# Optimization experiments

Measured on AMD Instinct MI355X. Metric: run time of the kernel, lower is better.

## Reference

```python
import jax, jax.numpy as jnp
import numpy as np

B, N, DIM = 16, 1024, 512
H, DH = 8, 64
INNER = H * DH            # 512
FF = 4 * DIM              # 2048
CIN = 2 * DIM             # conv inner dim = dim*expansion_factor = 1024
K = 31                    # depthwise kernel size
MAXPOS = 512
EPS = 1e-5


def layernorm(x, g, b):
    mu = jnp.mean(x, axis=-1, keepdims=True)
    var = jnp.mean(jnp.square(x - mu), axis=-1, keepdims=True)
    return (x - mu) * jax.lax.rsqrt(var + EPS) * g + b


def swish(x):
    return x * jax.nn.sigmoid(x)


def feed_forward(x, w1, b1, w2, b2):
    h = swish(x @ w1 + b1)
    return h @ w2 + b2


def setup_inputs() -> dict:
    key = jax.random.key(0)
    ks = jax.random.split(key, 16)
    s = 0.02
    w = lambda k, shape: (jax.random.normal(k, shape, jnp.float32) * s)
    inp = {
        "x": jax.random.normal(ks[0], (B, N, DIM), jnp.float32),
        # FF1
        "ff1_ln_g": jnp.ones((DIM,), jnp.float32), "ff1_ln_b": jnp.zeros((DIM,), jnp.float32),
        "ff1_w1": w(ks[1], (DIM, FF)), "ff1_b1": jnp.zeros((FF,), jnp.float32),
        "ff1_w2": w(ks[2], (FF, DIM)), "ff1_b2": jnp.zeros((DIM,), jnp.float32),
        # Attention (PreNorm)
        "attn_ln_g": jnp.ones((DIM,), jnp.float32), "attn_ln_b": jnp.zeros((DIM,), jnp.float32),
        "wq": w(ks[3], (DIM, INNER)),
        "wkv": w(ks[4], (DIM, 2 * INNER)),
        "wo": w(ks[5], (INNER, DIM)), "bo": jnp.zeros((DIM,), jnp.float32),
        "rel_emb": w(ks[6], (2 * MAXPOS + 1, DH)),
        # Conv module
        "conv_ln_g": jnp.ones((DIM,), jnp.float32), "conv_ln_b": jnp.zeros((DIM,), jnp.float32),
        "conv1_w": w(ks[7], (DIM, 2 * CIN)), "conv1_b": jnp.zeros((2 * CIN,), jnp.float32),
        "dw_w": w(ks[8], (CIN, 1, K)), "dw_b": jnp.zeros((CIN,), jnp.float32),
        "conv2_w": w(ks[9], (CIN, DIM)), "conv2_b": jnp.zeros((DIM,), jnp.float32),
        # FF2
        "ff2_ln_g": jnp.ones((DIM,), jnp.float32), "ff2_ln_b": jnp.zeros((DIM,), jnp.float32),
        "ff2_w1": w(ks[10], (DIM, FF)), "ff2_b1": jnp.zeros((FF,), jnp.float32),
        "ff2_w2": w(ks[11], (FF, DIM)), "ff2_b2": jnp.zeros((DIM,), jnp.float32),
        # post norm
        "post_ln_g": jnp.ones((DIM,), jnp.float32), "post_ln_b": jnp.zeros((DIM,), jnp.float32),
    }
    return inp


def attention(x, wq, wkv, wo, bo, rel_emb):
    b, n, _ = x.shape
    scale = DH ** -0.5
    q = (x @ wq).reshape(b, n, H, DH).transpose(0, 2, 1, 3)   # b h n d
    kv = x @ wkv
    k = kv[..., :INNER].reshape(b, n, H, DH).transpose(0, 2, 1, 3)
    v = kv[..., INNER:].reshape(b, n, H, DH).transpose(0, 2, 1, 3)
    dots = jnp.einsum("bhid,bhjd->bhij", q, k) * scale
    # relative positional bias via embedding lookup
    seq = jnp.arange(n)
    dist = jnp.clip(seq[:, None] - seq[None, :], -MAXPOS, MAXPOS) + MAXPOS  # [n, n]
    rel = jnp.take(rel_emb, dist, axis=0)                      # [n, n, d]
    pos = jnp.einsum("bhnd,njd->bhnj", q, rel) * scale
    attn = jax.nn.softmax(dots + pos, axis=-1)
    out = jnp.einsum("bhij,bhjd->bhid", attn, v)
    out = out.transpose(0, 2, 1, 3).reshape(b, n, INNER)
    return out @ wo + bo


def conv_module(x, ln_g, ln_b, conv1_w, conv1_b, dw_w, dw_b, conv2_w, conv2_b):
    h = layernorm(x, ln_g, ln_b)                               # [b, n, dim]
    h = h @ conv1_w + conv1_b                                  # pointwise conv -> [b, n, 2*CIN]
    a, g = h[..., :CIN], h[..., CIN:]
    h = a * jax.nn.sigmoid(g)                                  # GLU (channel dim)
    hc = h.transpose(0, 2, 1)                                  # [b, CIN, n]
    hc = jnp.pad(hc, ((0, 0), (0, 0), (K - 1, 0)))             # causal left pad
    hc = jax.lax.conv_general_dilated(
        hc, dw_w, window_strides=(1,), padding="VALID",
        feature_group_count=CIN, dimension_numbers=("NCH", "OIH", "NCH"),
    ) + dw_b[None, :, None]
    h = hc.transpose(0, 2, 1)                                  # [b, n, CIN]
    h = swish(h)
    return h @ conv2_w + conv2_b


def reference(x, ff1_ln_g, ff1_ln_b, ff1_w1, ff1_b1, ff1_w2, ff1_b2,
              attn_ln_g, attn_ln_b, wq, wkv, wo, bo, rel_emb,
              conv_ln_g, conv_ln_b, conv1_w, conv1_b, dw_w, dw_b, conv2_w, conv2_b,
              ff2_ln_g, ff2_ln_b, ff2_w1, ff2_b1, ff2_w2, ff2_b2,
              post_ln_g, post_ln_b):
    x = 0.5 * feed_forward(layernorm(x, ff1_ln_g, ff1_ln_b), ff1_w1, ff1_b1, ff1_w2, ff1_b2) + x
    x = attention(layernorm(x, attn_ln_g, attn_ln_b), wq, wkv, wo, bo, rel_emb) + x
    x = conv_module(x, conv_ln_g, conv_ln_b, conv1_w, conv1_b, dw_w, dw_b, conv2_w, conv2_b) + x
    x = 0.5 * feed_forward(layernorm(x, ff2_ln_g, ff2_ln_b), ff2_w1, ff2_b1, ff2_w2, ff2_b2) + x
    return layernorm(x, post_ln_g, post_ln_b)
```

## Files before the change

kernel.cpp:

```cpp
#include <hip/hip_runtime.h>


#define BN 16384

typedef unsigned short u16;
typedef __attribute__((ext_vector_type(8))) __bf16 bf16x8;
typedef __attribute__((ext_vector_type(4))) float f32x4;
typedef __attribute__((ext_vector_type(8))) unsigned short u16x8;

__device__ __forceinline__ float sigf(float x) { return 1.f / (1.f + __expf(-x)); }
__device__ __forceinline__ u16 f2bf(float f) {
  unsigned int u = __float_as_uint(f);
  u += 0x7FFF + ((u >> 16) & 1);
  return (u16)(u >> 16);
}
__device__ __forceinline__ u16 f2bfn(float f) {
  const __bf16 h = (__bf16)f;
  return __builtin_bit_cast(u16, h);
}
__device__ __forceinline__ float bf2f(u16 u) {
  return __uint_as_float(((unsigned int)u) << 16);
}
__device__ __forceinline__ void gl_lds16(const void* g, void* lds) {
  __builtin_amdgcn_global_load_lds(
      (const __attribute__((address_space(1))) unsigned int*)g,
      (__attribute__((address_space(3))) unsigned int*)lds, 16, 0, 0);
}

__global__ __launch_bounds__(256) void ln_kernel(const float* __restrict__ in,
    const float* __restrict__ g, const float* __restrict__ b,
    u16* outb, float* outf) {
  const int t = threadIdx.x;
  const int row = blockIdx.x * 2 + (t >> 7);
  const int tl = t & 127;
  const float4 v = ((const float4*)(in + (size_t)row * 512))[tl];
  float s = v.x + v.y + v.z + v.w;
  float sq = v.x * v.x + v.y * v.y + v.z * v.z + v.w * v.w;
#pragma unroll
  for (int o = 32; o > 0; o >>= 1) {
    s += __shfl_down(s, o);
    sq += __shfl_down(sq, o);
  }
  __shared__ float ss[4], ssq[4];
  if ((t & 63) == 0) { ss[t >> 6] = s; ssq[t >> 6] = sq; }
  __syncthreads();
  const int base = (t >> 7) * 2;
  s = ss[base] + ss[base + 1];
  sq = ssq[base] + ssq[base + 1];
  const float mu = s * (1.f / 512.f);
  const float var = fmaxf(sq * (1.f / 512.f) - mu * mu, 0.f);
  const float rstd = rsqrtf(var + 1e-5f);
  const float4 gg = ((const float4*)g)[tl];
  const float4 bb = ((const float4*)b)[tl];
  float o0 = (v.x - mu) * rstd * gg.x + bb.x;
  float o1 = (v.y - mu) * rstd * gg.y + bb.y;
  float o2 = (v.z - mu) * rstd * gg.z + bb.z;
  float o3 = (v.w - mu) * rstd * gg.w + bb.w;
  if (outf) {
    float4 o4 = {o0, o1, o2, o3};
    ((float4*)(outf + (size_t)row * 512))[tl] = o4;
  } else {
    ushort4 u4 = {f2bf(o0), f2bf(o1), f2bf(o2), f2bf(o3)};
    ((ushort4*)(outb + (size_t)row * 512))[tl] = u4;
  }
}

__global__ __launch_bounds__(256) void wtrans(const float* __restrict__ W,
                                              u16* __restrict__ WT, int K, int N) {
  const int n0 = blockIdx.x * 32, k0 = blockIdx.y * 32;
  const int t = threadIdx.x;
  const int tx = t & 31, ty = t >> 5;
  __shared__ float T[32][33];
#pragma unroll
  for (int i = 0; i < 4; ++i)
    T[tx][ty + 8 * i] = W[(size_t)(k0 + ty + 8 * i) * N + n0 + tx];
  __syncthreads();
#pragma unroll
  for (int i = 0; i < 4; ++i)
    WT[(size_t)(n0 + ty + 8 * i) * K + k0 + tx] = f2bf(T[ty + 8 * i][tx]);
}

__global__ __launch_bounds__(256) void cvt_bf16(const float* __restrict__ in,
                                                u16* __restrict__ out, int n) {
  const int i = blockIdx.x * 256 + threadIdx.x;
  if (i < n) out[i] = f2bf(in[i]);
}

__global__ __launch_bounds__(512) void gemm256(const u16* __restrict__ A,
    const u16* __restrict__ WT, const float* __restrict__ bias,
    u16* __restrict__ Cb, int K, int ldc, int act) {
  __shared__ __align__(16) u16 LDSB[65536];
  u16* const As0 = LDSB;
  u16* const As1 = LDSB + 16384;
  u16* const Bs0 = LDSB + 32768;
  u16* const Bs1 = LDSB + 49152;
  const int t = threadIdx.x;
  int bx = blockIdx.x, by = blockIdx.y;
  {
    const int nx = gridDim.x;
    const int lin = bx + nx * by;
    const int xcd = lin & 7;
    const int s = lin >> 3;
    const int ny8 = gridDim.y >> 3;
    const int sy = s / nx;
    by = xcd * ny8 + sy;
    bx = s - sy * nx;
  }
  const int n0 = bx * 256;
  const int m0 = by * 256;
  const int w = t >> 6;
  const int wr = w >> 2, wc = w & 3;
  const int lc = t & 15, lq = (t >> 4) & 3;

  f32x4 acc[8][4];
#pragma unroll
  for (int i = 0; i < 8; ++i)
#pragma unroll
    for (int j = 0; j < 4; ++j)
#pragma unroll
      for (int r = 0; r < 4; ++r) acc[i][j][r] = 0.f;

  int sfr[4], sfc[4];
#pragma unroll
  for (int s = 0; s < 4; ++s) {
    const int f = t + 512 * s;
    sfr[s] = f >> 3;
    sfc[s] = ((f & 7) ^ (sfr[s] & 7)) * 8;
  }

  auto STAGE = [&](u16* Ad, u16* Bd, int kt) {
#pragma unroll
    for (int s = 0; s < 4; ++s) {
      gl_lds16(&A[(size_t)(m0 + sfr[s]) * K + kt + sfc[s]], &Ad[(t + 512 * s) * 8]);
      gl_lds16(&WT[(size_t)(n0 + sfr[s]) * K + kt + sfc[s]], &Bd[(t + 512 * s) * 8]);
    }
  };

  auto COMPUTE = [&](const u16* Asrc, const u16* Bsrc) {
#pragma unroll
    for (int kk = 0; kk < 2; ++kk) {
      const int koff = ((kk * 4 + lq) ^ (lc & 7)) * 8;
      bf16x8 bfr[4];
#pragma unroll
      for (int j = 0; j < 4; ++j)
        bfr[j] = *(const bf16x8*)&Bsrc[(wc * 64 + j * 16 + lc) * 64 + koff];
#pragma unroll
      for (int i = 0; i < 8; ++i) {
        const bf16x8 af = *(const bf16x8*)&Asrc[(wr * 128 + i * 16 + lc) * 64 + koff];
#pragma unroll
        for (int j = 0; j < 4; ++j)
          acc[i][j] = __builtin_amdgcn_mfma_f32_16x16x32_bf16(af, bfr[j], acc[i][j], 0, 0, 0);
      }
    }
  };

  STAGE(As0, Bs0, 0);
  __syncthreads();

  for (int kt2 = 0; kt2 < K; kt2 += 128) {
    STAGE(As1, Bs1, kt2 + 64);
    COMPUTE(As0, Bs0);
    __syncthreads();
    if (kt2 + 128 < K) STAGE(As0, Bs0, kt2 + 128);
    COMPUTE(As1, Bs1);
    __syncthreads();
  }

#pragma unroll
  for (int j = 0; j < 4; ++j) {
    const int coll = wc * 64 + j * 16 + lc;
    const float bj = bias[n0 + coll];
#pragma unroll
    for (int i = 0; i < 8; ++i) {
      const int rowl0 = wr * 128 + i * 16 + lq * 4;
#pragma unroll
      for (int r = 0; r < 4; ++r) {
        float v = acc[i][j][r] + bj;
        if (act) v = v * sigf(v);
        LDSB[(rowl0 + r) * 256 + coll] = f2bfn(v);
      }
    }
  }
  __syncthreads();
#pragma unroll
  for (int vv = 0; vv < 16; ++vv) {
    const int e = t + 512 * vv;
    *(u16x8*)&Cb[(size_t)(m0 + (e >> 5)) * ldc + n0 + (e & 31) * 8] =
        *(const u16x8*)&LDSB[e * 8];
  }
}

__global__ __launch_bounds__(256) void gemm_bf16(const u16* __restrict__ A,
    const u16* __restrict__ WT, const float* __restrict__ bias,
    const float* res, float* Cf, u16* Cb, u16* VTout, int K, int N, int ldc,
    float alpha, int act, int qn, int vt0) {
  __shared__ __align__(16) u16 Ast[128 * 64];
  __shared__ __align__(16) u16 Bst[128 * 64];
  const int t = threadIdx.x;
  int bx = blockIdx.x, by = blockIdx.y;
  {
    const int nx = gridDim.x;
    const int lin = bx + nx * by;
    const int xcd = lin & 7;
    const int s = lin >> 3;
    const int ny8 = gridDim.y >> 3;
    const int sy = s / nx;
    by = xcd * ny8 + sy;
    bx = s - sy * nx;
  }
  const int n0 = bx * 128;
  const int m0 = by * 128;
  const int w = t >> 6;
  const int lc = t & 15, lq = (t >> 4) & 3;
  const int wy = w >> 1, wx = w & 1;
  f32x4 acc[4][4];
#pragma unroll
  for (int i = 0; i < 4; ++i)
#pragma unroll
    for (int j = 0; j < 4; ++j)
#pragma unroll
      for (int r = 0; r < 4; ++r) acc[i][j][r] = 0.f;

  const int koff0 = (lq ^ (lc & 7)) * 8;
  const int koff1 = ((4 + lq) ^ (lc & 7)) * 8;

  for (int kt = 0; kt < K; kt += 64) {
#pragma unroll
    for (int s = 0; s < 4; ++s) {
      const int f = t + 256 * s;
      const int fr = f >> 3;
      const int fc = (f & 7) ^ (fr & 7);
      gl_lds16(&A[(size_t)(m0 + fr) * K + kt + fc * 8], &Ast[f * 8]);
      gl_lds16(&WT[(size_t)(n0 + fr) * K + kt + fc * 8], &Bst[f * 8]);
    }
    __syncthreads();
#pragma unroll
    for (int kk = 0; kk < 2; ++kk) {
      const int koff = kk ? koff1 : koff0;
      bf16x8 bfr[4];
#pragma unroll
      for (int j = 0; j < 4; ++j)
        bfr[j] = *(const bf16x8*)&Bst[(wx * 64 + j * 16 + lc) * 64 + koff];
#pragma unroll
      for (int i = 0; i < 4; ++i) {
        const bf16x8 af = *(const bf16x8*)&Ast[(wy * 64 + i * 16 + lc) * 64 + koff];
#pragma unroll
        for (int j = 0; j < 4; ++j)
          acc[i][j] = __builtin_amdgcn_mfma_f32_16x16x32_bf16(af, bfr[j], acc[i][j], 0, 0, 0);
      }
    }
    __syncthreads();
  }

  const bool vtblk = (VTout != nullptr) && (n0 >= vt0);
  if (Cb && !vtblk) {
#pragma unroll
    for (int j = 0; j < 4; ++j) {
      const int coll = wx * 64 + j * 16 + lc;
      const float bj = bias ? bias[n0 + coll] : 0.f;
      const float al = ((n0 + coll) < qn) ? alpha : 1.f;
#pragma unroll
      for (int i = 0; i < 4; ++i) {
        const int rowl0 = wy * 64 + i * 16 + lq * 4;
#pragma unroll
        for (int r = 0; r < 4; ++r) {
          float v = acc[i][j][r] + bj;
          if (act) v = v * sigf(v);
          v *= al;
          const int rowl = rowl0 + r;
          u16* cl = (rowl < 64) ? &Ast[rowl * 128] : &Bst[(rowl - 64) * 128];
          cl[coll] = f2bfn(v);
        }
      }
    }
    __syncthreads();
#pragma unroll
    for (int vv = 0; vv < 8; ++vv) {
      const int e = t + 256 * vv;
      const int rowl = e >> 4;
      const int col = (e & 15) * 8;
      const u16* cl = (rowl < 64) ? &Ast[rowl * 128] : &Bst[(rowl - 64) * 128];
      const u16x8 val = *(const u16x8*)&cl[col];
      *(u16x8*)&Cb[(size_t)(m0 + rowl) * ldc + n0 + col] = val;
    }
    return;
  }

#pragma unroll
  for (int j = 0; j < 4; ++j) {
    const int col = n0 + wx * 64 + j * 16 + lc;
    const float bj = bias ? bias[col] : 0.f;
    const float al = (col < qn) ? alpha : 1.f;
    const bool vtc = vtblk && (col >= vt0);
#pragma unroll
    for (int i = 0; i < 4; ++i) {
      const int row0 = m0 + wy * 64 + i * 16 + lq * 4;
      float v4[4];
#pragma unroll
      for (int r = 0; r < 4; ++r) {
        float v = acc[i][j][r] + bj;
        if (act) v = v * sigf(v);
        v *= al;
        if (res) v += res[(size_t)(row0 + r) * ldc + col];
        v4[r] = v;
      }
      if (vtc) {
        const int cm = col - vt0;
        const int hh = cm >> 6, dd = cm & 63;
        const int bb = row0 >> 10, nl = row0 & 1023;
        ushort4 o4 = {f2bfn(v4[0]), f2bfn(v4[1]), f2bfn(v4[2]), f2bfn(v4[3])};
        *(ushort4*)&VTout[((size_t)((bb * 8 + hh) * 64 + dd)) * 1024 + nl] = o4;
      } else {
#pragma unroll
        for (int r = 0; r < 4; ++r) {
          const size_t off = (size_t)(row0 + r) * ldc + col;
          if (Cf) Cf[off] = v4[r];
          else Cb[off] = f2bfn(v4[r]);
        }
      }
    }
  }
}

__global__ __launch_bounds__(256) void attn_mfma(const u16* __restrict__ QKV,
    const u16* __restrict__ Vt, const u16* __restrict__ Rb, u16* __restrict__ O) {
  const int lin = blockIdx.x;
  const int hb = lin & 127;
  const int n0 = (lin >> 7) * 64;
  const int h = hb & 7, b = hb >> 3;
  const int t = threadIdx.x;
  const int w = t >> 6;
  const int lc = t & 15, lq = (t >> 4) & 3;

  __shared__ __align__(16) u16 Ks[2][64 * 64];
  __shared__ __align__(16) u16 Vs[2][64 * 64];
  __shared__ __align__(16) u16 SP[64 * 72];

  bf16x8 qf[2];
  {
    const size_t qrow = (size_t)(b * 1024 + n0 + w * 16 + lc) * 1536 + h * 64;
    qf[0] = *(const bf16x8*)&QKV[qrow + lq * 8];
    qf[1] = *(const bf16x8*)&QKV[qrow + 32 + lq * 8];
  }

  const u16* Kg = QKV + (size_t)b * 1024 * 1536 + 512 + h * 64;
  const u16* Vg = Vt + (size_t)(b * 8 + h) * 64 * 1024;

  const int srow = t >> 3;
  const int scb0 = ((t & 7) ^ (srow & 7)) * 8;
  const int srow1 = (t + 256) >> 3;
  const int scb1 = (((t + 256) & 7) ^ (srow1 & 7)) * 8;

  gl_lds16(&Kg[(size_t)srow * 1536 + scb0], &Ks[0][t * 8]);
  gl_lds16(&Vg[(size_t)srow * 1024 + scb0], &Vs[0][t * 8]);
  gl_lds16(&Kg[(size_t)srow1 * 1536 + scb1], &Ks[0][(t + 256) * 8]);
  gl_lds16(&Vg[(size_t)srow1 * 1024 + scb1], &Vs[0][(t + 256) * 8]);

  float l_r[4] = {0.f, 0.f, 0.f, 0.f};
  f32x4 o[4];
#pragma unroll
  for (int dt = 0; dt < 4; ++dt)
#pragma unroll
    for (int r = 0; r < 4; ++r) o[dt][r] = 0.f;

  const int swz0 = (lq ^ (lc & 7)) * 8;
  const int swz1 = ((4 + lq) ^ (lc & 7)) * 8;

  int buf = 0;
  for (int jt = 0; jt < 16; ++jt) {
    const int j0 = jt * 64;
    __syncthreads();

    if (jt < 15) {
      const int j1 = j0 + 64;
      gl_lds16(&Kg[(size_t)(j1 + srow) * 1536 + scb0], &Ks[buf ^ 1][t * 8]);
      gl_lds16(&Vg[(size_t)srow * 1024 + j1 + scb0], &Vs[buf ^ 1][t * 8]);
      gl_lds16(&Kg[(size_t)(j1 + srow1) * 1536 + scb1], &Ks[buf ^ 1][(t + 256) * 8]);
      gl_lds16(&Vg[(size_t)srow1 * 1024 + j1 + scb1], &Vs[buf ^ 1][(t + 256) * 8]);
    }

    f32x4 qk[4], pa[5];
#pragma unroll
    for (int j = 0; j < 4; ++j)
#pragma unroll
      for (int r = 0; r < 4; ++r) qk[j][r] = 0.f;
#pragma unroll
    for (int rtl = 0; rtl < 5; ++rtl)
#pragma unroll
      for (int r = 0; r < 4; ++r) pa[rtl][r] = 0.f;

    const int base = n0 - j0 - 63;
    const u16* rp[5];
#pragma unroll
    for (int rtl = 0; rtl < 5; ++rtl) {
      int p = base + (w + rtl) * 16 + lc;
      p = (p < -512 ? -512 : (p > 512 ? 512 : p)) + 512;
      rp[rtl] = Rb + (size_t)p * 64 + lq * 8;
    }

#pragma unroll
    for (int ks = 0; ks < 2; ++ks) {
      const int koff = ks ? swz1 : swz0;
      bf16x8 rfr[5];
#pragma unroll
      for (int rtl = 0; rtl < 5; ++rtl)
        rfr[rtl] = *(const bf16x8*)&rp[rtl][ks * 32];
#pragma unroll
      for (int j = 0; j < 4; ++j) {
        const bf16x8 bf = *(const bf16x8*)&Ks[buf][(j * 16 + lc) * 64 + koff];
        qk[j] = __builtin_amdgcn_mfma_f32_16x16x32_bf16(qf[ks], bf, qk[j], 0, 0, 0);
      }
#pragma unroll
      for (int rtl = 0; rtl < 5; ++rtl)
        pa[rtl] = __builtin_amdgcn_mfma_f32_16x16x32_bf16(qf[ks], rfr[rtl], pa[rtl], 0, 0, 0);
    }

#pragma unroll
    for (int rtl = 0; rtl < 5; ++rtl) {
      const int didx = (w + rtl) * 16 + lc;
#pragma unroll
      for (int r = 0; r < 4; ++r) {
        const int qr = w * 16 + lq * 4 + r;
        const int jc = qr - didx + 63;
        if ((unsigned)jc < 64u) SP[qr * 72 + jc] = f2bfn(pa[rtl][r]);
      }
    }

#pragma unroll
    for (int r = 0; r < 4; ++r) {
      const int qr = w * 16 + lq * 4 + r;
#pragma unroll
      for (int ti = 0; ti < 4; ++ti) {
        const int a = qr * 72 + ti * 16 + lc;
        const float e = exp2f(qk[ti][r] + bf2f(SP[a]));
        SP[a] = f2bfn(e);
        l_r[r] += e;
      }
    }

#pragma unroll
    for (int ks = 0; ks < 2; ++ks) {
      const bf16x8 af = *(const bf16x8*)&SP[(w * 16 + lc) * 72 + ks * 32 + lq * 8];
      const int koff = ks ? swz1 : swz0;
#pragma unroll
      for (int dt = 0; dt < 4; ++dt) {
        const bf16x8 bf = *(const bf16x8*)&Vs[buf][(dt * 16 + lc) * 64 + koff];
        o[dt] = __builtin_amdgcn_mfma_f32_16x16x32_bf16(af, bf, o[dt], 0, 0, 0);
      }
    }
    buf ^= 1;
  }

#pragma unroll
  for (int r = 0; r < 4; ++r) {
#pragma unroll
    for (int msk = 1; msk < 16; msk <<= 1) l_r[r] += __shfl_xor(l_r[r], msk);
  }

#pragma unroll
  for (int r = 0; r < 4; ++r) {
    const float inv = 1.f / l_r[r];
    const size_t row = (size_t)(b * 1024 + n0 + w * 16 + lq * 4 + r);
#pragma unroll
    for (int dt = 0; dt < 4; ++dt)
      O[row * 512 + h * 64 + dt * 16 + lc] = f2bfn(o[dt][r] * inv);
  }
}

__global__ __launch_bounds__(256) void dwconv_kernel(const u16* __restrict__ in,
    const float* __restrict__ w, const float* __restrict__ bias,
    u16* __restrict__ out) {
  const int n0 = blockIdx.x * 64;
  const int c0 = blockIdx.y * 64;
  const int b = blockIdx.z;
  const int t = threadIdx.x;
  __shared__ float hs[94][64];
  __shared__ float wsh[31][64];
  const int c = t & 63;
  const int g = t >> 6;
  for (int r = g; r < 94; r += 4) {
    const int n = n0 - 30 + r;
    float v = 0.f;
    if (n >= 0) {
      const size_t rowb = (size_t)(b * 1024 + n) * 2048;
      const float a = bf2f(in[rowb + c0 + c]);
      const float gg = bf2f(in[rowb + 1024 + c0 + c]);
      v = a * sigf(gg);
    }
    hs[r][c] = v;
  }
  for (int idx = t; idx < 31 * 64; idx += 256) {
    const int tap = idx >> 6, cc = idx & 63;
    wsh[tap][cc] = w[(size_t)(c0 + cc) * 31 + tap];
  }
  __syncthreads();
  float wr[31];
#pragma unroll
  for (int k = 0; k < 31; ++k) wr[k] = wsh[k][c];
  const float bsv = bias[c0 + c];
  float win[46];
  const int rbase = g * 16;
#pragma unroll
  for (int k = 0; k < 46; ++k) win[k] = hs[rbase + k][c];
#pragma unroll
  for (int i = 0; i < 16; ++i) {
    float acc = bsv;
#pragma unroll
    for (int k = 0; k < 31; ++k) acc += wr[k] * win[i + k];
    acc = acc * sigf(acc);
    out[(size_t)(b * 1024 + n0 + rbase + i) * 1024 + c0 + c] = f2bfn(acc);
  }
}

extern "C" void kernel_launch(void* const* d_in, const int* in_sizes, int n_in,
                              void* d_out, int out_size, void* d_ws, size_t ws_size,
                              hipStream_t stream) {
  const float* x        = (const float*)d_in[0];
  const float* ff1_ln_g = (const float*)d_in[1];
  const float* ff1_ln_b = (const float*)d_in[2];
  const float* ff1_w1   = (const float*)d_in[3];
  const float* ff1_b1   = (const float*)d_in[4];
  const float* ff1_w2   = (const float*)d_in[5];
  const float* ff1_b2   = (const float*)d_in[6];
  const float* attn_ln_g= (const float*)d_in[7];
  const float* attn_ln_b= (const float*)d_in[8];
  const float* wq       = (const float*)d_in[9];
  const float* wkv      = (const float*)d_in[10];
  const float* wo       = (const float*)d_in[11];
  const float* bo       = (const float*)d_in[12];
  const float* rel_emb  = (const float*)d_in[13];
  const float* conv_ln_g= (const float*)d_in[14];
  const float* conv_ln_b= (const float*)d_in[15];
  const float* conv1_w  = (const float*)d_in[16];
  const float* conv1_b  = (const float*)d_in[17];
  const float* dw_w     = (const float*)d_in[18];
  const float* dw_b     = (const float*)d_in[19];
  const float* conv2_w  = (const float*)d_in[20];
  const float* conv2_b  = (const float*)d_in[21];
  const float* ff2_ln_g = (const float*)d_in[22];
  const float* ff2_ln_b = (const float*)d_in[23];
  const float* ff2_w1   = (const float*)d_in[24];
  const float* ff2_b1   = (const float*)d_in[25];
  const float* ff2_w2   = (const float*)d_in[26];
  const float* ff2_b2   = (const float*)d_in[27];
  const float* post_ln_g= (const float*)d_in[28];
  const float* post_ln_b= (const float*)d_in[29];

  float* XRES = (float*)d_out;
  u16* ws = (u16*)d_ws;
  u16* LNB  = ws;
  u16* HID  = LNB + (size_t)BN * 512;
  u16* QKVB = HID + (size_t)BN * 2048;
  u16* VT   = QKVB + (size_t)BN * 1536;
  u16* DWB  = QKVB;
  u16* WTp = VT + (size_t)8192 * 1024;
  u16* wt_ff1w1 = WTp;                 WTp += (size_t)2048 * 512;
  u16* wt_ff1w2 = WTp;                 WTp += (size_t)512 * 2048;
  u16* wt_qkv   = WTp;                 WTp += (size_t)1536 * 512;
  u16* wt_wo    = WTp;                 WTp += (size_t)512 * 512;
  u16* wt_conv1 = WTp;                 WTp += (size_t)2048 * 512;
  u16* wt_conv2 = WTp;                 WTp += (size_t)512 * 1024;
  u16* wt_ff2w1 = WTp;                 WTp += (size_t)2048 * 512;
  u16* wt_ff2w2 = WTp;                 WTp += (size_t)512 * 2048;
  u16* RELB     = WTp;

  const dim3 blk(256);
  const float SC = 0.125f * 1.44269504f;

  wtrans<<<dim3(64, 16), blk, 0, stream>>>(ff1_w1, wt_ff1w1, 512, 2048);
  wtrans<<<dim3(16, 64), blk, 0, stream>>>(ff1_w2, wt_ff1w2, 2048, 512);
  wtrans<<<dim3(16, 16), blk, 0, stream>>>(wq, wt_qkv, 512, 512);
  wtrans<<<dim3(32, 16), blk, 0, stream>>>(wkv, wt_qkv + (size_t)512 * 512, 512, 1024);
  wtrans<<<dim3(16, 16), blk, 0, stream>>>(wo, wt_wo, 512, 512);
  wtrans<<<dim3(64, 16), blk, 0, stream>>>(conv1_w, wt_conv1, 512, 2048);
  wtrans<<<dim3(16, 32), blk, 0, stream>>>(conv2_w, wt_conv2, 1024, 512);
  wtrans<<<dim3(64, 16), blk, 0, stream>>>(ff2_w1, wt_ff2w1, 512, 2048);
  wtrans<<<dim3(16, 64), blk, 0, stream>>>(ff2_w2, wt_ff2w2, 2048, 512);
  cvt_bf16<<<257, blk, 0, stream>>>(rel_emb, RELB, 1025 * 64);

  ln_kernel<<<BN / 2, blk, 0, stream>>>(x, ff1_ln_g, ff1_ln_b, LNB, nullptr);
  gemm256<<<dim3(8, 64), dim3(512), 0, stream>>>(LNB, wt_ff1w1, ff1_b1, HID, 512, 2048, 1);
  gemm_bf16<<<dim3(4, 128), blk, 0, stream>>>(HID, wt_ff1w2, ff1_b2, x,
                                              XRES, nullptr, nullptr, 2048, 512, 512, 0.5f, 0, 512, 0);

  ln_kernel<<<BN / 2, blk, 0, stream>>>(XRES, attn_ln_g, attn_ln_b, LNB, nullptr);
  gemm_bf16<<<dim3(12, 128), blk, 0, stream>>>(LNB, wt_qkv, nullptr, nullptr,
                                               nullptr, QKVB, VT, 512, 1536, 1536, SC, 0, 512, 1024);
  attn_mfma<<<dim3(2048), blk, 0, stream>>>(QKVB, VT, RELB, LNB);
  gemm_bf16<<<dim3(4, 128), blk, 0, stream>>>(LNB, wt_wo, bo, XRES,
                                              XRES, nullptr, nullptr, 512, 512, 512, 1.f, 0, 512, 0);

  ln_kernel<<<BN / 2, blk, 0, stream>>>(XRES, conv_ln_g, conv_ln_b, LNB, nullptr);
  gemm256<<<dim3(8, 64), dim3(512), 0, stream>>>(LNB, wt_conv1, conv1_b, HID, 512, 2048, 0);
  dwconv_kernel<<<dim3(16, 16, 16), blk, 0, stream>>>(HID, dw_w, dw_b, DWB);
  gemm_bf16<<<dim3(4, 128), blk, 0, stream>>>(DWB, wt_conv2, conv2_b, XRES,
                                              XRES, nullptr, nullptr, 1024, 512, 512, 1.f, 0, 512, 0);

  ln_kernel<<<BN / 2, blk, 0, stream>>>(XRES, ff2_ln_g, ff2_ln_b, LNB, nullptr);
  gemm256<<<dim3(8, 64), dim3(512), 0, stream>>>(LNB, wt_ff2w1, ff2_b1, HID, 512, 2048, 1);
  gemm_bf16<<<dim3(4, 128), blk, 0, stream>>>(HID, wt_ff2w2, ff2_b2, XRES,
                                              XRES, nullptr, nullptr, 2048, 512, 512, 0.5f, 0, 512, 0);

  ln_kernel<<<BN / 2, blk, 0, stream>>>(XRES, post_ln_g, post_ln_b, nullptr, XRES);
}
```

Measured before the change: 862.7 us.

## Reuse relative-position fragment across key tiles, raise MFMA priority, vectorize dwconv loads

In the attention kernel, the fifth relative-embedding fragment of each key tile is taken from the first fragment loaded in the previous tile instead of being reloaded from global memory. This cuts one global load per ks step. s_setprio is raised around the two MFMA blocks so those waves get issue priority. The depthwise-conv staging loop now reads four bf16 values per thread as ushort4 and writes float4 into LDS, replacing scalar accesses. The reuse relies on the tile-to-tile overlap of the clamped position index, which needs the clamping at the edges to stay consistent.

```diff
diff --git a/kernel.cpp b/kernel.cpp
--- a/kernel.cpp
+++ b/kernel.cpp
@@ -366,6 +366,8 @@
   const int swz0 = (lq ^ (lc & 7)) * 8;
   const int swz1 = ((4 + lq) ^ (lc & 7)) * 8;
 
+  bf16x8 rsave[2];
+
   int buf = 0;
   for (int jt = 0; jt < 16; ++jt) {
     const int j0 = jt * 64;
@@ -390,30 +392,41 @@
       for (int r = 0; r < 4; ++r) pa[rtl][r] = 0.f;
 
     const int base = n0 - j0 - 63;
-    const u16* rp[5];
-#pragma unroll
-    for (int rtl = 0; rtl < 5; ++rtl) {
+    const u16* rp[4];
+#pragma unroll
+    for (int rtl = 0; rtl < 4; ++rtl) {
       int p = base + (w + rtl) * 16 + lc;
       p = (p < -512 ? -512 : (p > 512 ? 512 : p)) + 512;
       rp[rtl] = Rb + (size_t)p * 64 + lq * 8;
     }
-
+    const u16* rp4;
+    {
+      int p = base + (w + 4) * 16 + lc;
+      p = (p < -512 ? -512 : (p > 512 ? 512 : p)) + 512;
+      rp4 = Rb + (size_t)p * 64 + lq * 8;
+    }
+
+    __builtin_amdgcn_s_setprio(1);
 #pragma unroll
     for (int ks = 0; ks < 2; ++ks) {
       const int koff = ks ? swz1 : swz0;
-      bf16x8 rfr[5];
-#pragma unroll
-      for (int rtl = 0; rtl < 5; ++rtl)
+      bf16x8 rfr[4];
+#pragma unroll
+      for (int rtl = 0; rtl < 4; ++rtl)
         rfr[rtl] = *(const bf16x8*)&rp[rtl][ks * 32];
+      const bf16x8 rfr4 = (jt == 0) ? *(const bf16x8*)&rp4[ks * 32] : rsave[ks];
 #pragma unroll
       for (int j = 0; j < 4; ++j) {
         const bf16x8 bf = *(const bf16x8*)&Ks[buf][(j * 16 + lc) * 64 + koff];
         qk[j] = __builtin_amdgcn_mfma_f32_16x16x32_bf16(qf[ks], bf, qk[j], 0, 0, 0);
       }
 #pragma unroll
-      for (int rtl = 0; rtl < 5; ++rtl)
+      for (int rtl = 0; rtl < 4; ++rtl)
         pa[rtl] = __builtin_amdgcn_mfma_f32_16x16x32_bf16(qf[ks], rfr[rtl], pa[rtl], 0, 0, 0);
-    }
+      pa[4] = __builtin_amdgcn_mfma_f32_16x16x32_bf16(qf[ks], rfr4, pa[4], 0, 0, 0);
+      rsave[ks] = rfr[0];
+    }
+    __builtin_amdgcn_s_setprio(0);
 
 #pragma unroll
     for (int rtl = 0; rtl < 5; ++rtl) {
@@ -438,6 +451,7 @@
       }
     }
 
+    __builtin_amdgcn_s_setprio(1);
 #pragma unroll
     for (int ks = 0; ks < 2; ++ks) {
       const bf16x8 af = *(const bf16x8*)&SP[(w * 16 + lc) * 72 + ks * 32 + lq * 8];
@@ -448,6 +462,7 @@
         o[dt] = __builtin_amdgcn_mfma_f32_16x16x32_bf16(af, bf, o[dt], 0, 0, 0);
       }
     }
+    __builtin_amdgcn_s_setprio(0);
     buf ^= 1;
   }
 
@@ -478,16 +493,23 @@
   __shared__ float wsh[31][64];
   const int c = t & 63;
   const int g = t >> 6;
-  for (int r = g; r < 94; r += 4) {
-    const int n = n0 - 30 + r;
-    float v = 0.f;
-    if (n >= 0) {
-      const size_t rowb = (size_t)(b * 1024 + n) * 2048;
-      const float a = bf2f(in[rowb + c0 + c]);
-      const float gg = bf2f(in[rowb + 1024 + c0 + c]);
-      v = a * sigf(gg);
-    }
-    hs[r][c] = v;
+  {
+    const int cg = (t & 15) * 4;
+    const int rg = t >> 4;
+    for (int r = rg; r < 94; r += 16) {
+      const int n = n0 - 30 + r;
+      float4 v4 = {0.f, 0.f, 0.f, 0.f};
+      if (n >= 0) {
+        const size_t rowb = (size_t)(b * 1024 + n) * 2048;
+        const ushort4 a4 = *(const ushort4*)&in[rowb + c0 + cg];
+        const ushort4 g4 = *(const ushort4*)&in[rowb + 1024 + c0 + cg];
+        v4.x = bf2f(a4.x) * sigf(bf2f(g4.x));
+        v4.y = bf2f(a4.y) * sigf(bf2f(g4.y));
+        v4.z = bf2f(a4.z) * sigf(bf2f(g4.z));
+        v4.w = bf2f(a4.w) * sigf(bf2f(g4.w));
+      }
+      *(float4*)&hs[r][cg] = v4;
+    }
   }
   for (int idx = t; idx < 31 * 64; idx += 256) {
     const int tap = idx >> 6, cc = idx & 63;
```

After: 829.5 us. -3.8%, faster.
